# Performance work log

Measured on AMD Instinct MI355X. Metric: run time of the kernel, lower is better.

The kernel has to match this reference:

```python
import jax, jax.numpy as jnp
import numpy as np
from jax import lax


def setup_inputs() -> dict:
    key = jax.random.key(0)
    feature = jax.random.normal(key, (16, 64, 256, 256), dtype=jnp.float32)
    return {"feature": feature, "dist": 1}


def _avg_pool_up(feature):
    # avg_pool2d(k=3, stride=2, pad=1, count_include_pad=True): always divide by 9
    summed = lax.reduce_window(
        feature, 0.0, lax.add,
        window_dimensions=(1, 1, 3, 3),
        window_strides=(1, 1, 2, 2),
        padding=((0, 0), (0, 0), (1, 1), (1, 1)),
    )
    pooled = summed / 9.0  # [B, C, H/2, W/2]
    # nearest-neighbor upsample x2 back to [B, C, H, W]
    return jnp.repeat(jnp.repeat(pooled, 2, axis=2), 2, axis=3)


def reference(feature, dist):
    d = 2 * dist
    up = _avg_pool_up(feature)
    # order matches torch concat: top_left, top, top_right, left, right, bot_left, bot, bot_right
    shifts = [(d, d), (d, 0), (d, -d), (0, d), (0, -d), (-d, d), (-d, 0), (-d, -d)]
    diff = None
    for s in shifts:
        sq = jnp.sum((feature - jnp.roll(up, s, axis=(2, 3))) ** 2, axis=1, keepdims=True)
        diff = sq if diff is None else jnp.maximum(diff, sq)
    return diff  # [B, 1, H, W]
```

## Files before the change

### kernel.cpp

```cpp
#include <hip/hip_runtime.h>

__global__ __launch_bounds__(256) void pool_k(const float* __restrict__ f,
                                              float* __restrict__ pooled) {
    int idx = blockIdx.x * 256 + threadIdx.x;
    int j  = idx & 31;
    int py = (idx >> 5) & 127;
    int bc = idx >> 12;
    const float* fp = f + (size_t)bc * 65536;
    int y0 = 2 * py - 1;
    float s0 = 0.f, s1 = 0.f, s2 = 0.f, s3 = 0.f;
#pragma unroll
    for (int ky = 0; ky < 3; ++ky) {
        int y = y0 + ky;
        if ((unsigned)y < 256u) {
            const float* row = fp + y * 256 + 8 * j;
            float  e  = (j > 0) ? row[-1] : 0.f;
            float4 v0 = *(const float4*)(row);
            float4 v1 = *(const float4*)(row + 4);
            s0 += e    + v0.x + v0.y;
            s1 += v0.y + v0.z + v0.w;
            s2 += v0.w + v1.x + v1.y;
            s3 += v1.y + v1.z + v1.w;
        }
    }
    const float inv9 = 1.0f / 9.0f;
    float4 o = make_float4(s0 * inv9, s1 * inv9, s2 * inv9, s3 * inv9);
    *(float4*)(pooled + (size_t)bc * 16384 + py * 128 + 4 * j) = o;
}

__global__ __launch_bounds__(256) void diff_k(const float* __restrict__ f,
                                              const float* __restrict__ pooled,
                                              float* __restrict__ out,
                                              const int* __restrict__ distp) {
    int dist = *distp;
    int idx = blockIdx.x * 256 + threadIdx.x;
    int tx = idx & 127;
    int ty = (idx >> 7) & 127;
    int b  = idx >> 14;

    int pyv[3], pxv[3];
#pragma unroll
    for (int k = 0; k < 3; ++k) {
        int t = ty + (k - 1) * dist;
        t %= 128; if (t < 0) t += 128;
        pyv[k] = t;
        t = tx + (k - 1) * dist;
        t %= 128; if (t < 0) t += 128;
        pxv[k] = t;
    }

    const float* fb = f + (size_t)b * 64 * 65536;
    const float* pb = pooled + (size_t)b * 64 * 16384;
    int foff = (2 * ty) * 256 + 2 * tx;

    float dot[4][8], sp2[8], sf2[4];
#pragma unroll
    for (int q = 0; q < 4; ++q) { sf2[q] = 0.f;
#pragma unroll
        for (int n = 0; n < 8; ++n) dot[q][n] = 0.f; }
#pragma unroll
    for (int n = 0; n < 8; ++n) sp2[n] = 0.f;

    for (int c = 0; c < 64; ++c) {
        const float* fp = fb + (size_t)c * 65536 + foff;
        float2 r0 = *(const float2*)(fp);
        float2 r1 = *(const float2*)(fp + 256);
        float fv[4] = { r0.x, r0.y, r1.x, r1.y };

        const float* pp  = pb + (size_t)c * 16384;
        const float* pr0 = pp + pyv[0] * 128;
        const float* pr1 = pp + pyv[1] * 128;
        const float* pr2 = pp + pyv[2] * 128;
        float p[8];
        p[0] = pr0[pxv[0]]; p[1] = pr0[pxv[1]]; p[2] = pr0[pxv[2]];
        p[3] = pr1[pxv[0]];                     p[4] = pr1[pxv[2]];
        p[5] = pr2[pxv[0]]; p[6] = pr2[pxv[1]]; p[7] = pr2[pxv[2]];

#pragma unroll
        for (int n = 0; n < 8; ++n) sp2[n] = fmaf(p[n], p[n], sp2[n]);
#pragma unroll
        for (int q = 0; q < 4; ++q) {
            float fq = fv[q];
            sf2[q] = fmaf(fq, fq, sf2[q]);
#pragma unroll
            for (int n = 0; n < 8; ++n) dot[q][n] = fmaf(fq, p[n], dot[q][n]);
        }
    }

    float* ob = out + (size_t)b * 65536;
#pragma unroll
    for (int q = 0; q < 4; ++q) {
        float m = -3.4e38f;
#pragma unroll
        for (int n = 0; n < 8; ++n) {
            float v = fmaf(-2.f, dot[q][n], sf2[q] + sp2[n]);
            m = fmaxf(m, v);
        }
        int yy = 2 * ty + (q >> 1);
        int xx = 2 * tx + (q & 1);
        ob[yy * 256 + xx] = m;
    }
}

extern "C" void kernel_launch(void* const* d_in, const int* in_sizes, int n_in,
                              void* d_out, int out_size, void* d_ws, size_t ws_size,
                              hipStream_t stream) {
    const float* feature = (const float*)d_in[0];
    const int*   distp   = (const int*)d_in[1];
    float* out    = (float*)d_out;
    float* pooled = (float*)d_ws;

    pool_k<<<16384, 256, 0, stream>>>(feature, pooled);
    diff_k<<<1024, 256, 0, stream>>>(feature, pooled, out, distp);
}
```

Measured before the change: 427.4 us.

## Fuse pooling into diff kernel with per-band shared-memory pooled rows

Replaces the separate pool and diff kernels with one fused kernel. Each block handles a band of 4 pooled rows for one batch and recomputes the needed pooled rows (band plus halo) per channel into shared memory, then reads the shifted pooled neighbours from LDS. This removes the pooled intermediate's global write and read plus one launch. In exchange it adds two barriers per channel, recomputes halo rows, and launches only 512 blocks, which may limit occupancy and latency hiding. The MAXPR sizing also assumes dist is at most 5.

```diff
diff --git a/kernel.cpp b/kernel.cpp
--- a/kernel.cpp
+++ b/kernel.cpp
@@ -1,57 +1,35 @@
 #include <hip/hip_runtime.h>
 
-__global__ __launch_bounds__(256) void pool_k(const float* __restrict__ f,
-                                              float* __restrict__ pooled) {
-    int idx = blockIdx.x * 256 + threadIdx.x;
-    int j  = idx & 31;
-    int py = (idx >> 5) & 127;
-    int bc = idx >> 12;
-    const float* fp = f + (size_t)bc * 65536;
-    int y0 = 2 * py - 1;
-    float s0 = 0.f, s1 = 0.f, s2 = 0.f, s3 = 0.f;
-#pragma unroll
-    for (int ky = 0; ky < 3; ++ky) {
-        int y = y0 + ky;
-        if ((unsigned)y < 256u) {
-            const float* row = fp + y * 256 + 8 * j;
-            float  e  = (j > 0) ? row[-1] : 0.f;
-            float4 v0 = *(const float4*)(row);
-            float4 v1 = *(const float4*)(row + 4);
-            s0 += e    + v0.x + v0.y;
-            s1 += v0.y + v0.z + v0.w;
-            s2 += v0.w + v1.x + v1.y;
-            s3 += v1.y + v1.z + v1.w;
-        }
-    }
-    const float inv9 = 1.0f / 9.0f;
-    float4 o = make_float4(s0 * inv9, s1 * inv9, s2 * inv9, s3 * inv9);
-    *(float4*)(pooled + (size_t)bc * 16384 + py * 128 + 4 * j) = o;
-}
 
-__global__ __launch_bounds__(256) void diff_k(const float* __restrict__ f,
-                                              const float* __restrict__ pooled,
-                                              float* __restrict__ out,
-                                              const int* __restrict__ distp) {
-    int dist = *distp;
-    int idx = blockIdx.x * 256 + threadIdx.x;
-    int tx = idx & 127;
-    int ty = (idx >> 7) & 127;
-    int b  = idx >> 14;
+#define QR 4
+#define MAXPR (QR + 10)
 
-    int pyv[3], pxv[3];
-#pragma unroll
-    for (int k = 0; k < 3; ++k) {
-        int t = ty + (k - 1) * dist;
-        t %= 128; if (t < 0) t += 128;
-        pyv[k] = t;
-        t = tx + (k - 1) * dist;
-        t %= 128; if (t < 0) t += 128;
-        pxv[k] = t;
-    }
+__global__ __launch_bounds__(512) void fused_k(const float* __restrict__ f,
+                                               float* __restrict__ out,
+                                               const int* __restrict__ distp) {
+    __shared__ __align__(16) float ps[MAXPR][128];
+    const int dist = *distp;
+    const int PR   = QR + 2 * dist;
+
+    const int band = blockIdx.x & 31;
+    const int b    = blockIdx.x >> 5;
+    const int ty0  = band * QR;
+    const int tid  = threadIdx.x;
+    const int qr   = tid >> 7;
+    const int tx   = tid & 127;
+    const int ty   = ty0 + qr;
+
+    for (int w = tid; w < MAXPR * 128; w += 512) ((float*)ps)[w] = 0.f;
+    __syncthreads();
 
     const float* fb = f + (size_t)b * 64 * 65536;
-    const float* pb = pooled + (size_t)b * 64 * 16384;
-    int foff = (2 * ty) * 256 + 2 * tx;
+    const int foff = (2 * ty) * 256 + 2 * tx;
+
+    const int cxm = (tx - dist) & 127;
+    const int cxp = (tx + dist) & 127;
+    const int rm  = qr;
+    const int rc  = qr + dist;
+    const int rp  = qr + 2 * dist;
 
     float dot[4][8], sp2[8], sf2[4];
 #pragma unroll
@@ -62,19 +40,39 @@
     for (int n = 0; n < 8; ++n) sp2[n] = 0.f;
 
     for (int c = 0; c < 64; ++c) {
-        const float* fp = fb + (size_t)c * 65536 + foff;
-        float2 r0 = *(const float2*)(fp);
-        float2 r1 = *(const float2*)(fp + 256);
-        float fv[4] = { r0.x, r0.y, r1.x, r1.y };
+        const float* fc = fb + (size_t)c * 65536;
 
-        const float* pp  = pb + (size_t)c * 16384;
-        const float* pr0 = pp + pyv[0] * 128;
-        const float* pr1 = pp + pyv[1] * 128;
-        const float* pr2 = pp + pyv[2] * 128;
+        for (int w = tid; w < PR * 64; w += 512) {
+            int r = w >> 6;
+            int j = w & 63;
+            int pr = (ty0 - dist + r) & 127;
+            float s0 = 0.f, s1 = 0.f;
+            int y0 = 2 * pr - 1;
+#pragma unroll
+            for (int ky = 0; ky < 3; ++ky) {
+                int y = y0 + ky;
+                if ((unsigned)y < 256u) {
+                    const float* row = fc + y * 256 + 4 * j;
+                    float  e = (j > 0) ? row[-1] : 0.f;
+                    float4 v = *(const float4*)row;
+                    s0 += e   + v.x + v.y;
+                    s1 += v.y + v.z + v.w;
+                }
+            }
+            *(float2*)&ps[r][2 * j] =
+                make_float2(s0 * (1.f / 9.f), s1 * (1.f / 9.f));
+        }
+        __syncthreads();
+
+        const float* fp = fc + foff;
+        float2 q0 = *(const float2*)(fp);
+        float2 q1 = *(const float2*)(fp + 256);
+        float fv[4] = { q0.x, q0.y, q1.x, q1.y };
+
         float p[8];
-        p[0] = pr0[pxv[0]]; p[1] = pr0[pxv[1]]; p[2] = pr0[pxv[2]];
-        p[3] = pr1[pxv[0]];                     p[4] = pr1[pxv[2]];
-        p[5] = pr2[pxv[0]]; p[6] = pr2[pxv[1]]; p[7] = pr2[pxv[2]];
+        p[0] = ps[rm][cxm]; p[1] = ps[rm][tx]; p[2] = ps[rm][cxp];
+        p[3] = ps[rc][cxm];                    p[4] = ps[rc][cxp];
+        p[5] = ps[rp][cxm]; p[6] = ps[rp][tx]; p[7] = ps[rp][cxp];
 
 #pragma unroll
         for (int n = 0; n < 8; ++n) sp2[n] = fmaf(p[n], p[n], sp2[n]);
@@ -85,21 +83,21 @@
 #pragma unroll
             for (int n = 0; n < 8; ++n) dot[q][n] = fmaf(fq, p[n], dot[q][n]);
         }
+        __syncthreads();
     }
 
-    float* ob = out + (size_t)b * 65536;
+    float res[4];
 #pragma unroll
     for (int q = 0; q < 4; ++q) {
         float m = -3.4e38f;
 #pragma unroll
-        for (int n = 0; n < 8; ++n) {
-            float v = fmaf(-2.f, dot[q][n], sf2[q] + sp2[n]);
-            m = fmaxf(m, v);
-        }
-        int yy = 2 * ty + (q >> 1);
-        int xx = 2 * tx + (q & 1);
-        ob[yy * 256 + xx] = m;
+        for (int n = 0; n < 8; ++n)
+            m = fmaxf(m, fmaf(-2.f, dot[q][n], sf2[q] + sp2[n]));
+        res[q] = m;
     }
+    float* op = out + (size_t)b * 65536 + foff;
+    *(float2*)(op)       = make_float2(res[0], res[1]);
+    *(float2*)(op + 256) = make_float2(res[2], res[3]);
 }
 
 extern "C" void kernel_launch(void* const* d_in, const int* in_sizes, int n_in,
@@ -107,9 +105,7 @@
                               hipStream_t stream) {
     const float* feature = (const float*)d_in[0];
     const int*   distp   = (const int*)d_in[1];
-    float* out    = (float*)d_out;
-    float* pooled = (float*)d_ws;
+    float* out = (float*)d_out;
 
-    pool_k<<<16384, 256, 0, stream>>>(feature, pooled);
-    diff_k<<<1024, 256, 0, stream>>>(feature, pooled, out, distp);
+    fused_k<<<512, 512, 0, stream>>>(feature, out, distp);
 }
```

Result: faster. 416.5 us (-2.5%).
